# Optimization experiments

Hardware: AMD Instinct MI355X
Metric: run time of the kernel (lower is better)

## Reference

```python
import jax, jax.numpy as jnp
import numpy as np

D = 1024
H = 16
DH = D // H  # 64


def setup_inputs() -> dict:
    key = jax.random.key(0)
    ks = jax.random.split(key, 7)
    B, S = 2, 2048
    X = jax.random.normal(ks[0], (B, S, D), dtype=jnp.float32)
    s = 1.0 / np.sqrt(D)
    # per-head projection weights stacked over heads: [H, D, DH]
    Wq = jax.random.normal(ks[1], (H, D, DH), dtype=jnp.float32) * s
    Wk = jax.random.normal(ks[2], (H, D, DH), dtype=jnp.float32) * s
    Wv = jax.random.normal(ks[3], (H, D, DH), dtype=jnp.float32) * s
    bq = jax.random.normal(ks[4], (H, DH), dtype=jnp.float32) * s
    bk = jax.random.normal(ks[5], (H, DH), dtype=jnp.float32) * s
    bv = jax.random.normal(ks[6], (H, DH), dtype=jnp.float32) * s
    return {"X": X, "Wq": Wq, "Wk": Wk, "Wv": Wv, "bq": bq, "bk": bk, "bv": bv}


def reference(X, Wq, Wk, Wv, bq, bk, bv):
    B, S, _ = X.shape
    scale = jnp.sqrt(jnp.float32(DH))
    # per-head QKV projections, vectorized over heads: [B, H, S, DH]
    Q = jnp.einsum('bsd,hde->bhse', X, Wq) + bq[None, :, None, :]
    K = jnp.einsum('bsd,hde->bhse', X, Wk) + bk[None, :, None, :]
    V = jnp.einsum('bsd,hde->bhse', X, Wv) + bv[None, :, None, :]
    # full dense scores (the original materializes them): [B, H, S, S]
    QK = jnp.einsum('bhqe,bhke->bhqk', Q, K) / scale
    # NOTE: faithful to source — softmax over full row FIRST, then tril mask
    # applied AFTER softmax (rows are NOT renormalized).
    sQK = jax.nn.softmax(QK, axis=-1) * jnp.tril(jnp.ones((S, S), dtype=QK.dtype))
    Z = jnp.einsum('bhqk,bhke->bhqe', sQK, V)  # [B, H, S, DH]
    # concat heads along feature dim in head order
    return Z.transpose(0, 2, 1, 3).reshape(B, S, H * DH)
```

## Files before the change

### kernel.cpp

```cpp
#include <hip/hip_runtime.h>
#include <hip/hip_bf16.h>
#include <hip/hip_fp16.h>

#define DD   1024
#define HH   16
#define DHH  64
#define SS   2048
#define BB   2

using f32x4 = __attribute__((ext_vector_type(4))) float;
using s16x8 = __attribute__((ext_vector_type(8))) short;
using s16x4 = __attribute__((ext_vector_type(4))) short;
using f16x8 = __attribute__((ext_vector_type(8))) _Float16;

static __device__ __forceinline__ short f2h(float x) {
    _Float16 h = (_Float16)x;
    return __builtin_bit_cast(short, h);
}

static __device__ __forceinline__ void glds16(const void* g, void* l) {
    __builtin_amdgcn_global_load_lds(
        (const __attribute__((address_space(1))) unsigned int*)g,
        (__attribute__((address_space(3))) unsigned int*)l, 16, 0, 0);
}

static __device__ __forceinline__ int swz(int row, int blk) {
    return row * 128 + (((blk) ^ (row & 7)) << 4);
}

static __device__ __forceinline__ f32x4 MFMA16(s16x8 a, s16x8 b, f32x4 c) {
    return __builtin_amdgcn_mfma_f32_16x16x32_f16(
        __builtin_bit_cast(f16x8, a), __builtin_bit_cast(f16x8, b), c, 0, 0, 0);
}

#define WT_OFF 0u
#define VT_OFF 6291456u
#define QH_OFF 14680064u
#define KH_OFF 23068672u

__global__ __launch_bounds__(256, 2) void wsplit_kernel(
    const float* __restrict__ Wq, const float* __restrict__ Wk, const float* __restrict__ Wv,
    short* __restrict__ WtG)
{
    const int dt = blockIdx.x;
    const int mh = blockIdx.y;
    const int mat = mh >> 4, h = mh & 15;
    const int d0 = dt * 64;
    const float* Wm = (mat == 0 ? Wq : (mat == 1 ? Wk : Wv)) + (size_t)h * DD * DHH;

    __shared__ float Ws[64][65];
    const int t = threadIdx.x;

#pragma unroll
    for (int i = 0; i < 4; i++) {
        int f = t + 256 * i;
        int row = f >> 4;
        int c4  = f & 15;
        float4 v = *(const float4*)(Wm + (size_t)(d0 + row) * DHH + c4 * 4);
        Ws[row][c4 * 4 + 0] = v.x;
        Ws[row][c4 * 4 + 1] = v.y;
        Ws[row][c4 * 4 + 2] = v.z;
        Ws[row][c4 * 4 + 3] = v.w;
    }
    __syncthreads();

    const int e = t >> 2, dq = t & 3;
    s16x8 h0, h1;
#pragma unroll
    for (int i = 0; i < 8; i++) h0[i] = f2h(Ws[dq * 16 + i][e]);
#pragma unroll
    for (int i = 0; i < 8; i++) h1[i] = f2h(Ws[dq * 16 + 8 + i][e]);
    size_t off = ((size_t)(mh * 64 + e)) * DD + d0 + dq * 16;
    *(s16x8*)(WtG + off)     = h0;
    *(s16x8*)(WtG + off + 8) = h1;
}

__global__ __launch_bounds__(256, 2) void proj_qk_kernel(
    const float* __restrict__ X,
    const short* __restrict__ WtG,
    const float* __restrict__ bq, const float* __restrict__ bk,
    short* __restrict__ QhG, short* __restrict__ KhG)
{
    const int s0 = blockIdx.x * 128;
    const int n0 = blockIdx.y * 128;
    __shared__ __align__(16) char smem[32768];
    const int WT = 0, XT = 16384;

    const int t = threadIdx.x;
    const int w = t >> 6, lane = t & 63, g = lane >> 4, ln = lane & 15;
    const int wm = w >> 1, wn = w & 1;

    f32x4 acc[4][4];
#pragma unroll
    for (int i = 0; i < 4; i++)
#pragma unroll
        for (int j = 0; j < 4; j++) acc[i][j] = (f32x4){0.f, 0.f, 0.f, 0.f};

    for (int d0 = 0; d0 < DD; d0 += 64) {
        if (d0) __syncthreads();
#pragma unroll
        for (int p = 0; p < 4; p++) {
            int idx = p * 256 + t;
            int row = idx >> 3, blk = idx & 7;
            size_t so = (size_t)(n0 + row) * DD + d0 + ((blk ^ (row & 7)) * 8);
            glds16(WtG + so, smem + WT + idx * 16);
        }
#pragma unroll
        for (int p = 0; p < 4; p++) {
            int idx = p * 256 + t;
            int row = idx >> 3, blk = idx & 7;
            const float* xp = X + (size_t)(s0 + row) * DD + d0 + blk * 8;
            float4 va = *(const float4*)xp;
            float4 vb = *(const float4*)(xp + 4);
            float v[8] = {va.x, va.y, va.z, va.w, vb.x, vb.y, vb.z, vb.w};
            s16x8 hv;
#pragma unroll
            for (int i = 0; i < 8; i++) hv[i] = f2h(v[i]);
            *(s16x8*)(smem + XT + swz(row, blk)) = hv;
        }
        __syncthreads();

        s16x8 bx[4][2];
#pragma unroll
        for (int nf = 0; nf < 4; nf++)
#pragma unroll
            for (int kst = 0; kst < 2; kst++)
                bx[nf][kst] = *(const s16x8*)(smem + XT + swz(64 * wn + nf * 16 + ln, kst * 4 + g));
#pragma unroll
        for (int mf = 0; mf < 4; mf++) {
            s16x8 aw[2];
#pragma unroll
            for (int kst = 0; kst < 2; kst++)
                aw[kst] = *(const s16x8*)(smem + WT + swz(64 * wm + mf * 16 + ln, kst * 4 + g));
#pragma unroll
            for (int kst = 0; kst < 2; kst++)
#pragma unroll
                for (int nf = 0; nf < 4; nf++)
                    acc[mf][nf] = MFMA16(aw[kst], bx[nf][kst], acc[mf][nf]);
        }
    }

    const int mat = n0 >> 10;
    const int h = ((n0 + 64 * wm) >> 6) & 15;
    const float* bptr = (mat ? bk : bq) + h * 64;
    short* OutP = mat ? KhG : QhG;
    const float scale = mat ? 1.0f : 0.125f;

#pragma unroll
    for (int nf = 0; nf < 4; nf++) {
        int sg = s0 + 64 * wn + nf * 16 + ln;
        int bidx = sg >> 11, sr = sg & (SS - 1);
        size_t rowbase = ((size_t)((bidx * HH + h) * SS + sr)) * DHH;
#pragma unroll
        for (int mf = 0; mf < 4; mf++) {
            float4 bias = *(const float4*)(bptr + mf * 16 + g * 4);
            float bb[4] = {bias.x, bias.y, bias.z, bias.w};
            s16x4 h4;
#pragma unroll
            for (int r = 0; r < 4; r++) h4[r] = f2h((acc[mf][nf][r] + bb[r]) * scale);
            *(s16x4*)(OutP + rowbase + mf * 16 + g * 4) = h4;
        }
    }
}

__global__ __launch_bounds__(256, 2) void proj_v_kernel(
    const float* __restrict__ X,
    const short* __restrict__ WtG,
    const float* __restrict__ bv,
    short* __restrict__ VtG)
{
    const int s0 = blockIdx.x * 128;
    const int n0 = blockIdx.y * 128;
    __shared__ __align__(16) char smem[32768];
    const int XTo = 0, WTo = 16384;

    const int t = threadIdx.x;
    const int w = t >> 6, lane = t & 63, g = lane >> 4, ln = lane & 15;
    const int wm = w >> 1, wn = w & 1;

    f32x4 acc[4][4];
#pragma unroll
    for (int i = 0; i < 4; i++)
#pragma unroll
        for (int j = 0; j < 4; j++) acc[i][j] = (f32x4){0.f, 0.f, 0.f, 0.f};

    for (int d0 = 0; d0 < DD; d0 += 64) {
        if (d0) __syncthreads();
#pragma unroll
        for (int p = 0; p < 4; p++) {
            int idx = p * 256 + t;
            int row = idx >> 3, blk = idx & 7;
            size_t so = (size_t)(2048 + n0 + row) * DD + d0 + ((blk ^ (row & 7)) * 8);
            glds16(WtG + so, smem + WTo + idx * 16);
        }
#pragma unroll
        for (int p = 0; p < 4; p++) {
            int idx = p * 256 + t;
            int row = idx >> 3, blk = idx & 7;
            const float* xp = X + (size_t)(s0 + row) * DD + d0 + blk * 8;
            float4 va = *(const float4*)xp;
            float4 vb = *(const float4*)(xp + 4);
            float v[8] = {va.x, va.y, va.z, va.w, vb.x, vb.y, vb.z, vb.w};
            s16x8 hv;
#pragma unroll
            for (int i = 0; i < 8; i++) hv[i] = f2h(v[i]);
            *(s16x8*)(smem + XTo + swz(row, blk)) = hv;
        }
        __syncthreads();

        s16x8 bw[4][2];
#pragma unroll
        for (int nf = 0; nf < 4; nf++)
#pragma unroll
            for (int kst = 0; kst < 2; kst++)
                bw[nf][kst] = *(const s16x8*)(smem + WTo + swz(64 * wn + nf * 16 + ln, kst * 4 + g));
#pragma unroll
        for (int mf = 0; mf < 4; mf++) {
            s16x8 ax[2];
#pragma unroll
            for (int kst = 0; kst < 2; kst++)
                ax[kst] = *(const s16x8*)(smem + XTo + swz(64 * wm + mf * 16 + ln, kst * 4 + g));
#pragma unroll
            for (int kst = 0; kst < 2; kst++)
#pragma unroll
                for (int nf = 0; nf < 4; nf++)
                    acc[mf][nf] = MFMA16(ax[kst], bw[nf][kst], acc[mf][nf]);
        }
    }

    const int h = ((n0 + 64 * wn) >> 6) & 15;
#pragma unroll
    for (int nf = 0; nf < 4; nf++) {
        int e = nf * 16 + ln;
        float bvv = bv[h * 64 + e];
#pragma unroll
        for (int mf = 0; mf < 4; mf++) {
            int sgb = s0 + 64 * wm + mf * 16 + g * 4;
            int bidx = sgb >> 11, sr = sgb & (SS - 1);
            s16x4 v4;
#pragma unroll
            for (int r = 0; r < 4; r++) v4[r] = f2h(acc[mf][nf][r] + bvv);
            size_t base = ((size_t)(bidx * HH + h)) * (SS * DHH);
            int idx = ((((((sr >> 6) * 2 + ((sr >> 5) & 1)) * 4 + nf) * 4
                        + ((sr >> 3) & 3)) * 16 + ln) << 3) + (sr & 7);
            *(s16x4*)(VtG + base + idx) = v4;
        }
    }
}

__global__ __launch_bounds__(256, 4) void attn_kernel(
    const short* __restrict__ QhG, const short* __restrict__ KhG,
    const short* __restrict__ VtG,
    float* __restrict__ out)
{
    const int wid = (blockIdx.x & 7) * 128 + (blockIdx.x >> 3);
    const int qraw = wid & 31, h = (wid >> 5) & 15, b = wid >> 9;
    const int qt = ((wid >> 5) & 1) ? (31 - qraw) : qraw;
    const int q0 = qt * 64;
    const size_t ho = (size_t)(b * HH + h) * SS * DHH;

    __shared__ __align__(16) char smem[16384];

    const int t = threadIdx.x;
    const int w = t >> 6, lane = t & 63, g = lane >> 4, ln = lane & 15;
    const int qrow = 16 * w + ln;
    const int qg = q0 + qrow;

    s16x8 qh[2];
#pragma unroll
    for (int kst = 0; kst < 2; kst++)
        qh[kst] = *(const s16x8*)(QhG + ho + (size_t)qg * DHH + kst * 32 + g * 8);

    int soffA[2], krowA[2];
#pragma unroll
    for (int p = 0; p < 2; p++) {
        int idx = p * 256 + t;
        int row = idx >> 3, blk = idx & 7;
        soffA[p] = (blk ^ (row & 7)) * 8;
        krowA[p] = ((row >> 5) & 1) * 32 + ((row >> 2) & 3) * 8
                 + ((row >> 4) & 1) * 4 + (row & 3);
    }

    auto stageK = [&](int buf, int ktile) {
        const int k0s = ktile * 64;
#pragma unroll
        for (int p = 0; p < 2; p++) {
            int idx = p * 256 + t;
            glds16(KhG + ho + (size_t)(k0s + krowA[p]) * DHH + soffA[p],
                   smem + buf * 8192 + idx * 16);
        }
    };

    stageK(0, 0);

    f32x4 o[4];
#pragma unroll
    for (int i = 0; i < 4; i++) o[i] = (f32x4){0.f, 0.f, 0.f, 0.f};
    float lpart = 0.f;

    int cur = 0;
    for (int kt = 0; kt < SS / 64; kt++) {
        const int k0 = kt * 64;
        const bool do_pv = (kt <= qt);
        __syncthreads();

        s16x8 av[4][2];
        if (do_pv) {
#pragma unroll
            for (int mf = 0; mf < 4; mf++)
#pragma unroll
                for (int kst = 0; kst < 2; kst++)
                    av[mf][kst] = *(const s16x8*)(VtG + ho +
                        ((((((size_t)kt * 2 + kst) * 4 + mf) * 4 + g) * 16 + ln) << 3));
        }
        if (kt < SS / 64 - 1) stageK(cur ^ 1, kt + 1);

        f32x4 s[4];
#pragma unroll
        for (int i = 0; i < 4; i++) s[i] = (f32x4){0.f, 0.f, 0.f, 0.f};

        const char* Kb = smem + cur * 8192;
#pragma unroll
        for (int kst = 0; kst < 2; kst++) {
            s16x8 ak[4];
#pragma unroll
            for (int mf = 0; mf < 4; mf++)
                ak[mf] = *(const s16x8*)(Kb + swz(mf * 16 + ln, kst * 4 + g));
#pragma unroll
            for (int mf = 0; mf < 4; mf++)
                s[mf] = MFMA16(ak[mf], qh[kst], s[mf]);
        }

#pragma unroll
        for (int mf = 0; mf < 4; mf++)
#pragma unroll
            for (int r = 0; r < 4; r++)
                s[mf][r] = __expf(s[mf][r]);
        {
            float p0 = (s[0][0] + s[0][1]) + (s[0][2] + s[0][3]);
            float p1 = (s[1][0] + s[1][1]) + (s[1][2] + s[1][3]);
            float p2 = (s[2][0] + s[2][1]) + (s[2][2] + s[2][3]);
            float p3 = (s[3][0] + s[3][1]) + (s[3][2] + s[3][3]);
            lpart += (p0 + p1) + (p2 + p3);
        }

        if (do_pv) {
            const bool diag = (kt == qt);
#pragma unroll
            for (int kst = 0; kst < 2; kst++) {
                s16x8 bp;
                if (diag) {
                    int kb = k0 + kst * 32 + g * 8;
#pragma unroll
                    for (int r = 0; r < 4; r++) {
                        float pa = (kb + r     > qg) ? 0.f : s[2 * kst][r];
                        float pb = (kb + 4 + r > qg) ? 0.f : s[2 * kst + 1][r];
                        bp[r]     = f2h(pa);
                        bp[r + 4] = f2h(pb);
                    }
                } else {
#pragma unroll
                    for (int r = 0; r < 4; r++) {
                        bp[r]     = f2h(s[2 * kst][r]);
                        bp[r + 4] = f2h(s[2 * kst + 1][r]);
                    }
                }
#pragma unroll
                for (int mf = 0; mf < 4; mf++)
                    o[mf] = MFMA16(av[mf][kst], bp, o[mf]);
            }
        }
        cur ^= 1;
    }

    {
        float l = lpart;
        l += __shfl_xor(l, 16);
        l += __shfl_xor(l, 32);
        float inv = 1.0f / l;
        float* op = out + ((size_t)(b * SS + qg)) * (HH * DHH) + h * DHH;
#pragma unroll
        for (int mf = 0; mf < 4; mf++) {
            float4 vv = {o[mf][0] * inv, o[mf][1] * inv,
                         o[mf][2] * inv, o[mf][3] * inv};
            *(float4*)(op + mf * 16 + g * 4) = vv;
        }
    }
}

extern "C" void kernel_launch(void* const* d_in, const int* in_sizes, int n_in,
                              void* d_out, int out_size, void* d_ws, size_t ws_size,
                              hipStream_t stream) {
    const float* X  = (const float*)d_in[0];
    const float* Wq = (const float*)d_in[1];
    const float* Wk = (const float*)d_in[2];
    const float* Wv = (const float*)d_in[3];
    const float* bq = (const float*)d_in[4];
    const float* bk = (const float*)d_in[5];
    const float* bv = (const float*)d_in[6];
    float* out = (float*)d_out;

    char* wsb = (char*)d_ws;
    short* Wt = (short*)(wsb + WT_OFF);
    short* Vt = (short*)(wsb + VT_OFF);
    short* Qh = (short*)(wsb + QH_OFF);
    short* Kh = (short*)(wsb + KH_OFF);

    wsplit_kernel<<<dim3(16, 48), 256, 0, stream>>>(Wq, Wk, Wv, Wt);
    proj_qk_kernel<<<dim3(32, 16), 256, 0, stream>>>(X, Wt, bq, bk, Qh, Kh);
    proj_v_kernel<<<dim3(32, 8), 256, 0, stream>>>(X, Wt, bv, Vt);
    attn_kernel<<<1024, 256, 0, stream>>>(Qh, Kh, Vt, out);
}
```

Before: 106.9 us.

## Merge QKV projections into one launch, shrink attention tiles, use exp2 and packed conversion

The Q/K and V projection kernels are merged into a single grid of 24 column tiles that branches on the matrix index, removing one launch and letting all projection blocks share one wave. The attention kernel moves to 128-thread blocks covering 32 query rows, giving twice as many blocks for better load balance on the causal triangle. The softmax exponent becomes exp2, with the log2(e)/8 factor folded into the Q scale. The f16 conversion of P now uses packed round-toward-zero conversion. Smaller attention tiles mean K tiles are staged twice as often per query row, and the round-toward-zero rounding slightly changes numerics.

```diff
diff --git a/kernel.cpp b/kernel.cpp
--- a/kernel.cpp
+++ b/kernel.cpp
@@ -12,10 +12,21 @@
 using s16x8 = __attribute__((ext_vector_type(8))) short;
 using s16x4 = __attribute__((ext_vector_type(4))) short;
 using f16x8 = __attribute__((ext_vector_type(8))) _Float16;
+using u32x4 = __attribute__((ext_vector_type(4))) unsigned;
+
+#if __has_builtin(__builtin_amdgcn_exp2f)
+#define EXP2(x) __builtin_amdgcn_exp2f(x)
+#else
+#define EXP2(x) exp2f(x)
+#endif
 
 static __device__ __forceinline__ short f2h(float x) {
     _Float16 h = (_Float16)x;
     return __builtin_bit_cast(short, h);
+}
+static __device__ __forceinline__ unsigned pk2(float a, float b) {
+    auto h = __builtin_amdgcn_cvt_pkrtz(a, b);
+    return __builtin_bit_cast(unsigned, h);
 }
 
 static __device__ __forceinline__ void glds16(const void* g, void* l) {
@@ -32,6 +43,8 @@
     return __builtin_amdgcn_mfma_f32_16x16x32_f16(
         __builtin_bit_cast(f16x8, a), __builtin_bit_cast(f16x8, b), c, 0, 0, 0);
 }
+
+#define QSCALE 0.18033688011112042f
 
 #define WT_OFF 0u
 #define VT_OFF 6291456u
@@ -75,14 +88,16 @@
     *(s16x8*)(WtG + off + 8) = h1;
 }
 
-__global__ __launch_bounds__(256, 2) void proj_qk_kernel(
+__global__ __launch_bounds__(256, 2) void proj_kernel(
     const float* __restrict__ X,
     const short* __restrict__ WtG,
     const float* __restrict__ bq, const float* __restrict__ bk,
-    short* __restrict__ QhG, short* __restrict__ KhG)
+    const float* __restrict__ bv,
+    short* __restrict__ QhG, short* __restrict__ KhG, short* __restrict__ VtG)
 {
     const int s0 = blockIdx.x * 128;
     const int n0 = blockIdx.y * 128;
+    const int mat = n0 >> 10;
     __shared__ __align__(16) char smem[32768];
     const int WT = 0, XT = 16384;
 
@@ -120,143 +135,99 @@
         }
         __syncthreads();
 
-        s16x8 bx[4][2];
-#pragma unroll
-        for (int nf = 0; nf < 4; nf++)
-#pragma unroll
-            for (int kst = 0; kst < 2; kst++)
-                bx[nf][kst] = *(const s16x8*)(smem + XT + swz(64 * wn + nf * 16 + ln, kst * 4 + g));
-#pragma unroll
-        for (int mf = 0; mf < 4; mf++) {
-            s16x8 aw[2];
-#pragma unroll
-            for (int kst = 0; kst < 2; kst++)
-                aw[kst] = *(const s16x8*)(smem + WT + swz(64 * wm + mf * 16 + ln, kst * 4 + g));
-#pragma unroll
-            for (int kst = 0; kst < 2; kst++)
-#pragma unroll
-                for (int nf = 0; nf < 4; nf++)
-                    acc[mf][nf] = MFMA16(aw[kst], bx[nf][kst], acc[mf][nf]);
-        }
-    }
-
-    const int mat = n0 >> 10;
-    const int h = ((n0 + 64 * wm) >> 6) & 15;
-    const float* bptr = (mat ? bk : bq) + h * 64;
-    short* OutP = mat ? KhG : QhG;
-    const float scale = mat ? 1.0f : 0.125f;
-
-#pragma unroll
-    for (int nf = 0; nf < 4; nf++) {
-        int sg = s0 + 64 * wn + nf * 16 + ln;
-        int bidx = sg >> 11, sr = sg & (SS - 1);
-        size_t rowbase = ((size_t)((bidx * HH + h) * SS + sr)) * DHH;
-#pragma unroll
-        for (int mf = 0; mf < 4; mf++) {
-            float4 bias = *(const float4*)(bptr + mf * 16 + g * 4);
-            float bb[4] = {bias.x, bias.y, bias.z, bias.w};
-            s16x4 h4;
-#pragma unroll
-            for (int r = 0; r < 4; r++) h4[r] = f2h((acc[mf][nf][r] + bb[r]) * scale);
-            *(s16x4*)(OutP + rowbase + mf * 16 + g * 4) = h4;
-        }
-    }
-}
-
-__global__ __launch_bounds__(256, 2) void proj_v_kernel(
-    const float* __restrict__ X,
-    const short* __restrict__ WtG,
-    const float* __restrict__ bv,
-    short* __restrict__ VtG)
-{
-    const int s0 = blockIdx.x * 128;
-    const int n0 = blockIdx.y * 128;
-    __shared__ __align__(16) char smem[32768];
-    const int XTo = 0, WTo = 16384;
-
-    const int t = threadIdx.x;
-    const int w = t >> 6, lane = t & 63, g = lane >> 4, ln = lane & 15;
-    const int wm = w >> 1, wn = w & 1;
-
-    f32x4 acc[4][4];
-#pragma unroll
-    for (int i = 0; i < 4; i++)
-#pragma unroll
-        for (int j = 0; j < 4; j++) acc[i][j] = (f32x4){0.f, 0.f, 0.f, 0.f};
-
-    for (int d0 = 0; d0 < DD; d0 += 64) {
-        if (d0) __syncthreads();
-#pragma unroll
-        for (int p = 0; p < 4; p++) {
-            int idx = p * 256 + t;
-            int row = idx >> 3, blk = idx & 7;
-            size_t so = (size_t)(2048 + n0 + row) * DD + d0 + ((blk ^ (row & 7)) * 8);
-            glds16(WtG + so, smem + WTo + idx * 16);
-        }
-#pragma unroll
-        for (int p = 0; p < 4; p++) {
-            int idx = p * 256 + t;
-            int row = idx >> 3, blk = idx & 7;
-            const float* xp = X + (size_t)(s0 + row) * DD + d0 + blk * 8;
-            float4 va = *(const float4*)xp;
-            float4 vb = *(const float4*)(xp + 4);
-            float v[8] = {va.x, va.y, va.z, va.w, vb.x, vb.y, vb.z, vb.w};
-            s16x8 hv;
-#pragma unroll
-            for (int i = 0; i < 8; i++) hv[i] = f2h(v[i]);
-            *(s16x8*)(smem + XTo + swz(row, blk)) = hv;
-        }
-        __syncthreads();
-
-        s16x8 bw[4][2];
-#pragma unroll
-        for (int nf = 0; nf < 4; nf++)
-#pragma unroll
-            for (int kst = 0; kst < 2; kst++)
-                bw[nf][kst] = *(const s16x8*)(smem + WTo + swz(64 * wn + nf * 16 + ln, kst * 4 + g));
-#pragma unroll
-        for (int mf = 0; mf < 4; mf++) {
-            s16x8 ax[2];
-#pragma unroll
-            for (int kst = 0; kst < 2; kst++)
-                ax[kst] = *(const s16x8*)(smem + XTo + swz(64 * wm + mf * 16 + ln, kst * 4 + g));
-#pragma unroll
-            for (int kst = 0; kst < 2; kst++)
-#pragma unroll
-                for (int nf = 0; nf < 4; nf++)
-                    acc[mf][nf] = MFMA16(ax[kst], bw[nf][kst], acc[mf][nf]);
-        }
-    }
-
-    const int h = ((n0 + 64 * wn) >> 6) & 15;
-#pragma unroll
-    for (int nf = 0; nf < 4; nf++) {
-        int e = nf * 16 + ln;
-        float bvv = bv[h * 64 + e];
-#pragma unroll
-        for (int mf = 0; mf < 4; mf++) {
-            int sgb = s0 + 64 * wm + mf * 16 + g * 4;
-            int bidx = sgb >> 11, sr = sgb & (SS - 1);
-            s16x4 v4;
-#pragma unroll
-            for (int r = 0; r < 4; r++) v4[r] = f2h(acc[mf][nf][r] + bvv);
-            size_t base = ((size_t)(bidx * HH + h)) * (SS * DHH);
-            int idx = ((((((sr >> 6) * 2 + ((sr >> 5) & 1)) * 4 + nf) * 4
-                        + ((sr >> 3) & 3)) * 16 + ln) << 3) + (sr & 7);
-            *(s16x4*)(VtG + base + idx) = v4;
-        }
-    }
-}
-
-__global__ __launch_bounds__(256, 4) void attn_kernel(
+        if (mat < 2) {
+            s16x8 bx[4][2];
+#pragma unroll
+            for (int nf = 0; nf < 4; nf++)
+#pragma unroll
+                for (int kst = 0; kst < 2; kst++)
+                    bx[nf][kst] = *(const s16x8*)(smem + XT + swz(64 * wn + nf * 16 + ln, kst * 4 + g));
+#pragma unroll
+            for (int mf = 0; mf < 4; mf++) {
+                s16x8 aw[2];
+#pragma unroll
+                for (int kst = 0; kst < 2; kst++)
+                    aw[kst] = *(const s16x8*)(smem + WT + swz(64 * wm + mf * 16 + ln, kst * 4 + g));
+#pragma unroll
+                for (int kst = 0; kst < 2; kst++)
+#pragma unroll
+                    for (int nf = 0; nf < 4; nf++)
+                        acc[mf][nf] = MFMA16(aw[kst], bx[nf][kst], acc[mf][nf]);
+            }
+        } else {
+            s16x8 bw[4][2];
+#pragma unroll
+            for (int nf = 0; nf < 4; nf++)
+#pragma unroll
+                for (int kst = 0; kst < 2; kst++)
+                    bw[nf][kst] = *(const s16x8*)(smem + WT + swz(64 * wn + nf * 16 + ln, kst * 4 + g));
+#pragma unroll
+            for (int mf = 0; mf < 4; mf++) {
+                s16x8 ax[2];
+#pragma unroll
+                for (int kst = 0; kst < 2; kst++)
+                    ax[kst] = *(const s16x8*)(smem + XT + swz(64 * wm + mf * 16 + ln, kst * 4 + g));
+#pragma unroll
+                for (int kst = 0; kst < 2; kst++)
+#pragma unroll
+                    for (int nf = 0; nf < 4; nf++)
+                        acc[mf][nf] = MFMA16(ax[kst], bw[nf][kst], acc[mf][nf]);
+            }
+        }
+    }
+
+    if (mat < 2) {
+        const int h = ((n0 + 64 * wm) >> 6) & 15;
+        const float* bptr = (mat ? bk : bq) + h * 64;
+        short* OutP = mat ? KhG : QhG;
+        const float scale = mat ? 1.0f : QSCALE;
+#pragma unroll
+        for (int nf = 0; nf < 4; nf++) {
+            int sg = s0 + 64 * wn + nf * 16 + ln;
+            int bidx = sg >> 11, sr = sg & (SS - 1);
+            size_t rowbase = ((size_t)((bidx * HH + h) * SS + sr)) * DHH;
+#pragma unroll
+            for (int mf = 0; mf < 4; mf++) {
+                float4 bias = *(const float4*)(bptr + mf * 16 + g * 4);
+                float bb[4] = {bias.x, bias.y, bias.z, bias.w};
+                s16x4 h4;
+#pragma unroll
+                for (int r = 0; r < 4; r++) h4[r] = f2h((acc[mf][nf][r] + bb[r]) * scale);
+                *(s16x4*)(OutP + rowbase + mf * 16 + g * 4) = h4;
+            }
+        }
+    } else {
+        const int h = ((n0 + 64 * wn) >> 6) & 15;
+#pragma unroll
+        for (int nf = 0; nf < 4; nf++) {
+            int e = nf * 16 + ln;
+            float bvv = bv[h * 64 + e];
+#pragma unroll
+            for (int mf = 0; mf < 4; mf++) {
+                int sgb = s0 + 64 * wm + mf * 16 + g * 4;
+                int bidx = sgb >> 11, sr = sgb & (SS - 1);
+                s16x4 v4;
+#pragma unroll
+                for (int r = 0; r < 4; r++) v4[r] = f2h(acc[mf][nf][r] + bvv);
+                size_t base = ((size_t)(bidx * HH + h)) * (SS * DHH);
+                int idx = ((((((sr >> 6) * 2 + ((sr >> 5) & 1)) * 4 + nf) * 4
+                            + ((sr >> 3) & 3)) * 16 + ln) << 3) + (sr & 7);
+                *(s16x4*)(VtG + base + idx) = v4;
+            }
+        }
+    }
+}
+
+__global__ __launch_bounds__(128, 4) void attn_kernel(
     const short* __restrict__ QhG, const short* __restrict__ KhG,
     const short* __restrict__ VtG,
     float* __restrict__ out)
 {
-    const int wid = (blockIdx.x & 7) * 128 + (blockIdx.x >> 3);
-    const int qraw = wid & 31, h = (wid >> 5) & 15, b = wid >> 9;
-    const int qt = ((wid >> 5) & 1) ? (31 - qraw) : qraw;
-    const int q0 = qt * 64;
+    const int wid = (blockIdx.x & 7) * 256 + (blockIdx.x >> 3);
+    const int qraw = wid & 63, h = (wid >> 6) & 15, b = wid >> 10;
+    const int qt = ((wid >> 6) & 1) ? (63 - qraw) : qraw;
+    const int q0 = qt * 32;
+    const int ktd = qt >> 1;
     const size_t ho = (size_t)(b * HH + h) * SS * DHH;
 
     __shared__ __align__(16) char smem[16384];
@@ -271,10 +242,10 @@
     for (int kst = 0; kst < 2; kst++)
         qh[kst] = *(const s16x8*)(QhG + ho + (size_t)qg * DHH + kst * 32 + g * 8);
 
-    int soffA[2], krowA[2];
-#pragma unroll
-    for (int p = 0; p < 2; p++) {
-        int idx = p * 256 + t;
+    int soffA[4], krowA[4];
+#pragma unroll
+    for (int p = 0; p < 4; p++) {
+        int idx = p * 128 + t;
         int row = idx >> 3, blk = idx & 7;
         soffA[p] = (blk ^ (row & 7)) * 8;
         krowA[p] = ((row >> 5) & 1) * 32 + ((row >> 2) & 3) * 8
@@ -284,8 +255,8 @@
     auto stageK = [&](int buf, int ktile) {
         const int k0s = ktile * 64;
 #pragma unroll
-        for (int p = 0; p < 2; p++) {
-            int idx = p * 256 + t;
+        for (int p = 0; p < 4; p++) {
+            int idx = p * 128 + t;
             glds16(KhG + ho + (size_t)(k0s + krowA[p]) * DHH + soffA[p],
                    smem + buf * 8192 + idx * 16);
         }
@@ -301,7 +272,7 @@
     int cur = 0;
     for (int kt = 0; kt < SS / 64; kt++) {
         const int k0 = kt * 64;
-        const bool do_pv = (kt <= qt);
+        const bool do_pv = (kt <= ktd);
         __syncthreads();
 
         s16x8 av[4][2];
@@ -335,7 +306,7 @@
         for (int mf = 0; mf < 4; mf++)
 #pragma unroll
             for (int r = 0; r < 4; r++)
-                s[mf][r] = __expf(s[mf][r]);
+                s[mf][r] = EXP2(s[mf][r]);
         {
             float p0 = (s[0][0] + s[0][1]) + (s[0][2] + s[0][3]);
             float p1 = (s[1][0] + s[1][1]) + (s[1][2] + s[1][3]);
@@ -345,26 +316,27 @@
         }
 
         if (do_pv) {
-            const bool diag = (kt == qt);
+            const bool diag = (kt == ktd);
 #pragma unroll
             for (int kst = 0; kst < 2; kst++) {
-                s16x8 bp;
+                u32x4 u;
                 if (diag) {
                     int kb = k0 + kst * 32 + g * 8;
+                    float pa[4], pb[4];
 #pragma unroll
                     for (int r = 0; r < 4; r++) {
-                        float pa = (kb + r     > qg) ? 0.f : s[2 * kst][r];
-                        float pb = (kb + 4 + r > qg) ? 0.f : s[2 * kst + 1][r];
-                        bp[r]     = f2h(pa);
-                        bp[r + 4] = f2h(pb);
+                        pa[r] = (kb + r     > qg) ? 0.f : s[2 * kst][r];
+                        pb[r] = (kb + 4 + r > qg) ? 0.f : s[2 * kst + 1][r];
                     }
+                    u.x = pk2(pa[0], pa[1]); u.y = pk2(pa[2], pa[3]);
+                    u.z = pk2(pb[0], pb[1]); u.w = pk2(pb[2], pb[3]);
                 } else {
-#pragma unroll
-                    for (int r = 0; r < 4; r++) {
-                        bp[r]     = f2h(s[2 * kst][r]);
-                        bp[r + 4] = f2h(s[2 * kst + 1][r]);
-                    }
+                    u.x = pk2(s[2 * kst][0], s[2 * kst][1]);
+                    u.y = pk2(s[2 * kst][2], s[2 * kst][3]);
+                    u.z = pk2(s[2 * kst + 1][0], s[2 * kst + 1][1]);
+                    u.w = pk2(s[2 * kst + 1][2], s[2 * kst + 1][3]);
                 }
+                s16x8 bp = __builtin_bit_cast(s16x8, u);
 #pragma unroll
                 for (int mf = 0; mf < 4; mf++)
                     o[mf] = MFMA16(av[mf][kst], bp, o[mf]);
@@ -407,7 +379,6 @@
     short* Kh = (short*)(wsb + KH_OFF);
 
     wsplit_kernel<<<dim3(16, 48), 256, 0, stream>>>(Wq, Wk, Wv, Wt);
-    proj_qk_kernel<<<dim3(32, 16), 256, 0, stream>>>(X, Wt, bq, bk, Qh, Kh);
-    proj_v_kernel<<<dim3(32, 8), 256, 0, stream>>>(X, Wt, bv, Vt);
-    attn_kernel<<<1024, 256, 0, stream>>>(Qh, Kh, Vt, out);
-}
+    proj_kernel<<<dim3(32, 24), 256, 0, stream>>>(X, Wt, bq, bk, bv, Qh, Kh, Vt);
+    attn_kernel<<<2048, 128, 0, stream>>>(Qh, Kh, Vt, out);
+}
```

Result: slower. 125.5 us (+17.4%).
